# Kernel tuning notes

Measured on AMD Instinct MI355X. Metric: run time of the kernel, lower is better.

Reference implementation:

```python
import jax, jax.numpy as jnp
import numpy as np

N = 768       # num nodes
E = 12288     # num edges (avg degree 16)
D_IN = 6
H = 256       # hidden_dim
TEMPERATURE = 1.0


def gcn_conv(x, W, b, src, dst, n):
    """PyG GCNConv: add self-loops, symmetric deg^-1/2 normalization, then xW aggregation + bias."""
    h = x @ W  # [n, H]
    loop = jnp.arange(n, dtype=src.dtype)
    s = jnp.concatenate([src, loop])
    d = jnp.concatenate([dst, loop])
    deg = jax.ops.segment_sum(jnp.ones(s.shape, dtype=h.dtype), d, num_segments=n)
    dinv = jnp.where(deg > 0, jax.lax.rsqrt(deg), 0.0)
    norm = dinv[s] * dinv[d]  # [E+n]
    out = jax.ops.segment_sum(h[s] * norm[:, None], d, num_segments=n)
    return out + b


def setup_inputs() -> dict:
    key = jax.random.key(0)
    ks = jax.random.split(key, 10)
    sc = lambda fan: np.float32(1.0 / np.sqrt(fan))
    x = jax.random.normal(ks[0], (N, D_IN), jnp.float32)
    edge_index = jax.random.randint(ks[1], (2, E), 0, N, dtype=jnp.int32)
    Wc1 = jax.random.normal(ks[2], (D_IN, H), jnp.float32) * sc(D_IN)
    bc1 = jnp.zeros((H,), jnp.float32)
    Wc2 = jax.random.normal(ks[3], (H, H), jnp.float32) * sc(H)
    bc2 = jnp.zeros((H,), jnp.float32)
    We1 = jax.random.normal(ks[4], (2 * H, H), jnp.float32) * sc(2 * H)
    be1 = jax.random.normal(ks[5], (H,), jnp.float32) * sc(2 * H)
    We2 = jax.random.normal(ks[6], (H, 1), jnp.float32) * sc(H)
    be2 = jax.random.normal(ks[7], (1,), jnp.float32) * sc(H)
    return {"x": x, "edge_index": edge_index, "Wc1": Wc1, "bc1": bc1,
            "Wc2": Wc2, "bc2": bc2, "We1": We1, "be1": be1, "We2": We2, "be2": be2}


def reference(x, edge_index, Wc1, bc1, Wc2, bc2, We1, be1, We2, be2):
    src, dst = edge_index[0], edge_index[1]
    h = jax.nn.elu(gcn_conv(x, Wc1, bc1, src, dst, N))
    h = gcn_conv(h, Wc2, bc2, src, dst, N)  # [N, H]
    # edge scorer: Linear(cat([x_i, x_j])) == x_i @ We1[:H] + x_j @ We1[H:] + be1
    ai = h @ We1[:H]   # [N, H], contribution of x_i (row node)
    aj = h @ We1[H:]   # [N, H], contribution of x_j (col node)
    pair = jax.nn.relu(ai[:, None, :] + aj[None, :, :] + be1)  # [N, N, H]
    logits = jnp.einsum('ijh,h->ij', pair, We2[:, 0]) + be2[0]  # [N, N]
    logits = logits / TEMPERATURE
    logits = jnp.where(jnp.eye(N, dtype=bool), -jnp.inf, logits)
    return jax.nn.softmax(logits, axis=-1)
```

## Files before the change

### kernel.cpp

```cpp
#include <hip/hip_runtime.h>
#include <math.h>

#define N_NODES 768
#define N_EDGES 12288
#define D_INF 6
#define H 256
#define CAP 128
#define LC 256

__global__ __launch_bounds__(256) void k_prep(
    const float* __restrict__ x, const int* __restrict__ ei,
    const float* __restrict__ Wc1, const float* __restrict__ bc1,
    int* __restrict__ cnt_g, int* __restrict__ slots, float* __restrict__ h1) {
    __shared__ int s_cnt[N_NODES];
    __shared__ int s_list[LC];
    __shared__ int s_nm, s_pos[3];
    __shared__ float s_agg[3][D_INF];
    const int t = threadIdx.x, b = blockIdx.x, v0 = b * 3;
    const int* src = ei;
    const int* dst = ei + N_EDGES;

    for (int v = t; v < N_NODES; v += 256) s_cnt[v] = 0;
    if (t == 0) s_nm = 0;
    if (t < 3) s_pos[t] = 0;
    if (t < 3 * D_INF) ((float*)s_agg)[t] = 0.f;
    __syncthreads();
    for (int e = t; e < N_EDGES; e += 256) {
        int d = dst[e];
        atomicAdd(&s_cnt[d], 1);
        unsigned li = (unsigned)(d - v0);
        if (li < 3u) {
            int p = atomicAdd(&s_nm, 1);
            if (p < LC) s_list[p] = (src[e] << 2) | (int)li;
        }
    }
    __syncthreads();
    const int nm = min(s_nm, LC);
    if (t < 3) cnt_g[v0 + t] = s_cnt[v0 + t];
    for (int m = t; m < nm; m += 256) {
        int pk = s_list[m];
        int s = pk >> 2, li = pk & 3;
        int p = atomicAdd(&s_pos[li], 1);
        if (p < CAP) slots[(v0 + li) * CAP + p] = s;
        float w = rsqrtf((float)(s_cnt[s] + 1)) * rsqrtf((float)(s_cnt[v0 + li] + 1));
        #pragma unroll
        for (int k = 0; k < D_INF; ++k)
            atomicAdd(&s_agg[li][k], w * x[s * D_INF + k]);
    }
    if (t < 3) {
        int v = v0 + t;
        float dv2 = 1.0f / (float)(s_cnt[v] + 1);
        #pragma unroll
        for (int k = 0; k < D_INF; ++k)
            atomicAdd(&s_agg[t][k], dv2 * x[v * D_INF + k]);
    }
    __syncthreads();
    #pragma unroll
    for (int r = 0; r < 3; ++r) {
        float acc = bc1[t];
        #pragma unroll
        for (int k = 0; k < D_INF; ++k)
            acc = fmaf(s_agg[r][k], Wc1[k * H + t], acc);
        h1[(v0 + r) * H + t] = (acc > 0.f) ? acc : expm1f(acc);
    }
}

__global__ __launch_bounds__(256) void k_agg(
    const float* __restrict__ h1, const int* __restrict__ cnt,
    const int* __restrict__ slots, float* __restrict__ agg2) {
    __shared__ int   s_s[CAP];
    __shared__ float s_w[CAP];
    const int v = blockIdx.x, t = threadIdx.x;
    const int c = cnt[v];
    const int cc = min(c, CAP);
    const float dv = rsqrtf((float)(c + 1));
    for (int i = t; i < cc; i += 256) {
        int s = slots[v * CAP + i];
        s_s[i] = s;
        s_w[i] = rsqrtf((float)(cnt[s] + 1)) * dv;
    }
    __syncthreads();
    float acc = dv * dv * h1[v * H + t];
    #pragma unroll 4
    for (int n = 0; n < cc; ++n)
        acc = fmaf(s_w[n], h1[s_s[n] * H + t], acc);
    agg2[v * H + t] = acc;
}

__global__ __launch_bounds__(1024) void k_h2(
    const float* __restrict__ agg2, const float* __restrict__ Wc2,
    const float* __restrict__ bc2, float* __restrict__ h2) {
    __shared__ __align__(16) float s_part[16][3][H];
    const int t = threadIdx.x, b = blockIdx.x;
    const int lane = t & 63, w = t >> 6;
    const int v0 = b * 3, k0 = w * 16;

    float a[3][16];
    #pragma unroll
    for (int r = 0; r < 3; ++r)
        #pragma unroll
        for (int q = 0; q < 4; ++q) {
            float4 v = *(const float4*)(agg2 + (size_t)(v0 + r) * H + k0 + q * 4);
            a[r][q * 4 + 0] = v.x; a[r][q * 4 + 1] = v.y;
            a[r][q * 4 + 2] = v.z; a[r][q * 4 + 3] = v.w;
        }
    float4 c0 = {0.f, 0.f, 0.f, 0.f}, c1 = c0, c2 = c0;
    #pragma unroll
    for (int kk = 0; kk < 16; ++kk) {
        float4 wv = *(const float4*)(Wc2 + (size_t)(k0 + kk) * H + (lane << 2));
        c0.x = fmaf(a[0][kk], wv.x, c0.x); c0.y = fmaf(a[0][kk], wv.y, c0.y);
        c0.z = fmaf(a[0][kk], wv.z, c0.z); c0.w = fmaf(a[0][kk], wv.w, c0.w);
        c1.x = fmaf(a[1][kk], wv.x, c1.x); c1.y = fmaf(a[1][kk], wv.y, c1.y);
        c1.z = fmaf(a[1][kk], wv.z, c1.z); c1.w = fmaf(a[1][kk], wv.w, c1.w);
        c2.x = fmaf(a[2][kk], wv.x, c2.x); c2.y = fmaf(a[2][kk], wv.y, c2.y);
        c2.z = fmaf(a[2][kk], wv.z, c2.z); c2.w = fmaf(a[2][kk], wv.w, c2.w);
    }
    *(float4*)&s_part[w][0][lane << 2] = c0;
    *(float4*)&s_part[w][1][lane << 2] = c1;
    *(float4*)&s_part[w][2][lane << 2] = c2;
    __syncthreads();
    if (t < 3 * H) {
        int r = t >> 8, c = t & 255;
        float v = bc2[c];
        #pragma unroll
        for (int ww = 0; ww < 16; ++ww) v += s_part[ww][r][c];
        h2[(size_t)(v0 + r) * H + c] = v;
    }
}

__global__ __launch_bounds__(1024) void k_ae(
    const float* __restrict__ h2, const float* __restrict__ We1,
    const float* __restrict__ be1, float* __restrict__ aib,
    float* __restrict__ ajcT) {
    __shared__ __align__(16) float s_part[16][6][H];
    const int t = threadIdx.x, b = blockIdx.x;
    const int lane = t & 63, w = t >> 6;
    const int v0 = b * 3, k0 = w * 16;

    float a[3][16];
    #pragma unroll
    for (int r = 0; r < 3; ++r)
        #pragma unroll
        for (int q = 0; q < 4; ++q) {
            float4 v = *(const float4*)(h2 + (size_t)(v0 + r) * H + k0 + q * 4);
            a[r][q * 4 + 0] = v.x; a[r][q * 4 + 1] = v.y;
            a[r][q * 4 + 2] = v.z; a[r][q * 4 + 3] = v.w;
        }
    float4 ca0 = {0.f, 0.f, 0.f, 0.f}, ca1 = ca0, ca2 = ca0;
    float4 cb0 = ca0, cb1 = ca0, cb2 = ca0;
    #pragma unroll
    for (int kk = 0; kk < 16; ++kk) {
        int k = k0 + kk;
        float4 wa = *(const float4*)(We1 + (size_t)k * H + (lane << 2));
        float4 wb = *(const float4*)(We1 + (size_t)(H + k) * H + (lane << 2));
        ca0.x = fmaf(a[0][kk], wa.x, ca0.x); ca0.y = fmaf(a[0][kk], wa.y, ca0.y);
        ca0.z = fmaf(a[0][kk], wa.z, ca0.z); ca0.w = fmaf(a[0][kk], wa.w, ca0.w);
        ca1.x = fmaf(a[1][kk], wa.x, ca1.x); ca1.y = fmaf(a[1][kk], wa.y, ca1.y);
        ca1.z = fmaf(a[1][kk], wa.z, ca1.z); ca1.w = fmaf(a[1][kk], wa.w, ca1.w);
        ca2.x = fmaf(a[2][kk], wa.x, ca2.x); ca2.y = fmaf(a[2][kk], wa.y, ca2.y);
        ca2.z = fmaf(a[2][kk], wa.z, ca2.z); ca2.w = fmaf(a[2][kk], wa.w, ca2.w);
        cb0.x = fmaf(a[0][kk], wb.x, cb0.x); cb0.y = fmaf(a[0][kk], wb.y, cb0.y);
        cb0.z = fmaf(a[0][kk], wb.z, cb0.z); cb0.w = fmaf(a[0][kk], wb.w, cb0.w);
        cb1.x = fmaf(a[1][kk], wb.x, cb1.x); cb1.y = fmaf(a[1][kk], wb.y, cb1.y);
        cb1.z = fmaf(a[1][kk], wb.z, cb1.z); cb1.w = fmaf(a[1][kk], wb.w, cb1.w);
        cb2.x = fmaf(a[2][kk], wb.x, cb2.x); cb2.y = fmaf(a[2][kk], wb.y, cb2.y);
        cb2.z = fmaf(a[2][kk], wb.z, cb2.z); cb2.w = fmaf(a[2][kk], wb.w, cb2.w);
    }
    *(float4*)&s_part[w][0][lane << 2] = ca0;
    *(float4*)&s_part[w][1][lane << 2] = ca1;
    *(float4*)&s_part[w][2][lane << 2] = ca2;
    *(float4*)&s_part[w][3][lane << 2] = cb0;
    *(float4*)&s_part[w][4][lane << 2] = cb1;
    *(float4*)&s_part[w][5][lane << 2] = cb2;
    __syncthreads();
    for (int idx = t; idx < 6 * H; idx += 1024) {
        int q = idx >> 8, c = idx & 255;
        float v = 0.f;
        #pragma unroll
        for (int ww = 0; ww < 16; ++ww) v += s_part[ww][q][c];
        if (q < 3) aib[(size_t)(v0 + q) * H + c] = v;
        else       ajcT[(size_t)c * N_NODES + v0 + (q - 3)] = v + be1[c];
    }
}

__global__ __launch_bounds__(512) void k_pair2(
    const float* __restrict__ aib, const float* __restrict__ ajcT,
    const float* __restrict__ We2, float* __restrict__ out) {
    __shared__ float s_ai[3 * H];
    __shared__ float s_w2[H];
    __shared__ __align__(16) float s_p[8 * 3 * N_NODES];
    __shared__ float s_lg[3 * N_NODES];
    __shared__ float red[3 * 256];
    const int t = threadIdx.x, b = blockIdx.x;
    const int lane = t & 63, w = t >> 6;
    const int i0 = b * 3, h0 = w * 32;

    for (int i = t; i < 3 * H; i += 512)
        s_ai[i] = aib[(size_t)(i0 + (i >> 8)) * H + (i & 255)];
    if (t < H) s_w2[t] = We2[t];
    __syncthreads();

    float4 acc[3][3];
    #pragma unroll
    for (int r = 0; r < 3; ++r)
        #pragma unroll
        for (int jj = 0; jj < 3; ++jj)
            acc[r][jj] = make_float4(0.f, 0.f, 0.f, 0.f);

    #pragma unroll 4
    for (int hh = 0; hh < 32; ++hh) {
        int h = h0 + hh;
        float wv = s_w2[h];
        float a0 = s_ai[h], a1 = s_ai[H + h], a2 = s_ai[2 * H + h];
        const float* col = ajcT + (size_t)h * N_NODES + (lane << 2);
        #pragma unroll
        for (int jj = 0; jj < 3; ++jj) {
            float4 bv = *(const float4*)(col + jj * 256);
            acc[0][jj].x = fmaf(fmaxf(a0 + bv.x, 0.f), wv, acc[0][jj].x);
            acc[0][jj].y = fmaf(fmaxf(a0 + bv.y, 0.f), wv, acc[0][jj].y);
            acc[0][jj].z = fmaf(fmaxf(a0 + bv.z, 0.f), wv, acc[0][jj].z);
            acc[0][jj].w = fmaf(fmaxf(a0 + bv.w, 0.f), wv, acc[0][jj].w);
            acc[1][jj].x = fmaf(fmaxf(a1 + bv.x, 0.f), wv, acc[1][jj].x);
            acc[1][jj].y = fmaf(fmaxf(a1 + bv.y, 0.f), wv, acc[1][jj].y);
            acc[1][jj].z = fmaf(fmaxf(a1 + bv.z, 0.f), wv, acc[1][jj].z);
            acc[1][jj].w = fmaf(fmaxf(a1 + bv.w, 0.f), wv, acc[1][jj].w);
            acc[2][jj].x = fmaf(fmaxf(a2 + bv.x, 0.f), wv, acc[2][jj].x);
            acc[2][jj].y = fmaf(fmaxf(a2 + bv.y, 0.f), wv, acc[2][jj].y);
            acc[2][jj].z = fmaf(fmaxf(a2 + bv.z, 0.f), wv, acc[2][jj].z);
            acc[2][jj].w = fmaf(fmaxf(a2 + bv.w, 0.f), wv, acc[2][jj].w);
        }
    }
    #pragma unroll
    for (int r = 0; r < 3; ++r)
        #pragma unroll
        for (int jj = 0; jj < 3; ++jj)
            *(float4*)&s_p[(w * 3 + r) * N_NODES + jj * 256 + (lane << 2)] = acc[r][jj];
    __syncthreads();

    for (int idx = t; idx < 3 * N_NODES; idx += 512) {
        int r = idx / N_NODES, j = idx - r * N_NODES;
        float v = 0.f;
        #pragma unroll
        for (int ww = 0; ww < 8; ++ww) v += s_p[(ww * 3 + r) * N_NODES + j];
        s_lg[idx] = (j == i0 + r) ? -INFINITY : v;
    }
    __syncthreads();

    const int tc = t & 255, th = t >> 8;
    if (th == 0) {
        red[tc] = fmaxf(fmaxf(s_lg[tc], s_lg[tc + 256]), s_lg[tc + 512]);
        red[512 + tc] = fmaxf(fmaxf(s_lg[1536 + tc], s_lg[1536 + tc + 256]),
                              s_lg[1536 + tc + 512]);
    } else {
        red[256 + tc] = fmaxf(fmaxf(s_lg[768 + tc], s_lg[768 + tc + 256]),
                              s_lg[768 + tc + 512]);
    }
    __syncthreads();
    for (int s = 128; s > 0; s >>= 1) {
        if (th == 0 && tc < s) {
            red[tc] = fmaxf(red[tc], red[tc + s]);
            red[512 + tc] = fmaxf(red[512 + tc], red[512 + tc + s]);
        } else if (th == 1 && tc < s) {
            red[256 + tc] = fmaxf(red[256 + tc], red[256 + tc + s]);
        }
        __syncthreads();
    }
    float mx0 = red[0], mx1 = red[256], mx2 = red[512];
    __syncthreads();
    if (th == 0) {
        red[tc] = __expf(s_lg[tc] - mx0) + __expf(s_lg[tc + 256] - mx0)
                + __expf(s_lg[tc + 512] - mx0);
        red[512 + tc] = __expf(s_lg[1536 + tc] - mx2) + __expf(s_lg[1536 + tc + 256] - mx2)
                      + __expf(s_lg[1536 + tc + 512] - mx2);
    } else {
        red[256 + tc] = __expf(s_lg[768 + tc] - mx1) + __expf(s_lg[768 + tc + 256] - mx1)
                      + __expf(s_lg[768 + tc + 512] - mx1);
    }
    __syncthreads();
    for (int s = 128; s > 0; s >>= 1) {
        if (th == 0 && tc < s) {
            red[tc] += red[tc + s];
            red[512 + tc] += red[512 + tc + s];
        } else if (th == 1 && tc < s) {
            red[256 + tc] += red[256 + tc + s];
        }
        __syncthreads();
    }
    float iv0 = 1.0f / red[0], iv1 = 1.0f / red[256], iv2 = 1.0f / red[512];

    for (int idx = t; idx < 3 * N_NODES; idx += 512) {
        int r = idx / N_NODES, j = idx - r * N_NODES;
        float m = (r == 0) ? mx0 : (r == 1) ? mx1 : mx2;
        float iv = (r == 0) ? iv0 : (r == 1) ? iv1 : iv2;
        out[(size_t)(i0 + r) * N_NODES + j] = __expf(s_lg[idx] - m) * iv;
    }
}

extern "C" void kernel_launch(void* const* d_in, const int* in_sizes, int n_in,
                              void* d_out, int out_size, void* d_ws, size_t ws_size,
                              hipStream_t stream) {
    const float* x   = (const float*)d_in[0];
    const int*   ei  = (const int*)d_in[1];
    const float* Wc1 = (const float*)d_in[2];
    const float* bc1 = (const float*)d_in[3];
    const float* Wc2 = (const float*)d_in[4];
    const float* bc2 = (const float*)d_in[5];
    const float* We1 = (const float*)d_in[6];
    const float* be1 = (const float*)d_in[7];
    const float* We2 = (const float*)d_in[8];
    float* out = (float*)d_out;

    char* ws = (char*)d_ws;
    int*   cnt  = (int*)(ws + 0);
    int*   slots= (int*)(ws + 4096);
    float* h1   = (float*)(ws + 397312);
    float* agg2 = (float*)(ws + 1183744);
    float* h2   = (float*)(ws + 1970176);
    float* aib  = (float*)(ws + 2756608);
    float* ajcT = (float*)(ws + 3543040);

    k_prep<<<N_NODES / 3, 256, 0, stream>>>(x, ei, Wc1, bc1, cnt, slots, h1);
    k_agg<<<N_NODES, 256, 0, stream>>>(h1, cnt, slots, agg2);
    k_h2<<<N_NODES / 3, 1024, 0, stream>>>(agg2, Wc2, bc2, h2);
    k_ae<<<N_NODES / 3, 1024, 0, stream>>>(h2, We1, be1, aib, ajcT);
    k_pair2<<<N_NODES / 3, 512, 0, stream>>>(aib, ajcT, We2, out);
}
```

Before: 54.68 us.

## Fuse aggregation, Wc2 GEMM and edge projection into one kernel

Merges the second-layer neighbor aggregation, the Wc2 matmul and the We1 projections into a single kernel with 1024 threads per block, each block handling 3 nodes. Intermediates (aggregated features and h2) stay in shared memory instead of going through global buffers. This removes two kernel launches and the global round trips for agg2 and h2. In exchange, the aggregation phase now runs with only 768 of 1024 threads active and 256 blocks instead of 768, and shared memory use per block grows.

```diff
diff --git a/kernel.cpp b/kernel.cpp
--- a/kernel.cpp
+++ b/kernel.cpp
@@ -65,121 +65,131 @@
     }
 }
 
-__global__ __launch_bounds__(256) void k_agg(
+__global__ __launch_bounds__(1024) void k_mid(
     const float* __restrict__ h1, const int* __restrict__ cnt,
-    const int* __restrict__ slots, float* __restrict__ agg2) {
-    __shared__ int   s_s[CAP];
-    __shared__ float s_w[CAP];
-    const int v = blockIdx.x, t = threadIdx.x;
-    const int c = cnt[v];
-    const int cc = min(c, CAP);
-    const float dv = rsqrtf((float)(c + 1));
-    for (int i = t; i < cc; i += 256) {
-        int s = slots[v * CAP + i];
-        s_s[i] = s;
-        s_w[i] = rsqrtf((float)(cnt[s] + 1)) * dv;
-    }
-    __syncthreads();
-    float acc = dv * dv * h1[v * H + t];
-    #pragma unroll 4
-    for (int n = 0; n < cc; ++n)
-        acc = fmaf(s_w[n], h1[s_s[n] * H + t], acc);
-    agg2[v * H + t] = acc;
-}
-
-__global__ __launch_bounds__(1024) void k_h2(
-    const float* __restrict__ agg2, const float* __restrict__ Wc2,
-    const float* __restrict__ bc2, float* __restrict__ h2) {
-    __shared__ __align__(16) float s_part[16][3][H];
+    const int* __restrict__ slots, const float* __restrict__ Wc2,
+    const float* __restrict__ bc2, const float* __restrict__ We1,
+    const float* __restrict__ be1, float* __restrict__ aib,
+    float* __restrict__ ajcT) {
+    __shared__ int   s_s[3][CAP];
+    __shared__ float s_w[3][CAP];
+    __shared__ int   s_cc[3];
+    __shared__ float s_dv[3];
+    __shared__ __align__(16) float s_agg[3][H];
+    __shared__ __align__(16) float s_h2[3][H];
+    __shared__ __align__(16) float s_part[16][6][H];
     const int t = threadIdx.x, b = blockIdx.x;
+    const int q = t >> 8, tc = t & 255;
     const int lane = t & 63, w = t >> 6;
     const int v0 = b * 3, k0 = w * 16;
 
-    float a[3][16];
-    #pragma unroll
-    for (int r = 0; r < 3; ++r)
-        #pragma unroll
-        for (int q = 0; q < 4; ++q) {
-            float4 v = *(const float4*)(agg2 + (size_t)(v0 + r) * H + k0 + q * 4);
-            a[r][q * 4 + 0] = v.x; a[r][q * 4 + 1] = v.y;
-            a[r][q * 4 + 2] = v.z; a[r][q * 4 + 3] = v.w;
-        }
-    float4 c0 = {0.f, 0.f, 0.f, 0.f}, c1 = c0, c2 = c0;
-    #pragma unroll
-    for (int kk = 0; kk < 16; ++kk) {
-        float4 wv = *(const float4*)(Wc2 + (size_t)(k0 + kk) * H + (lane << 2));
-        c0.x = fmaf(a[0][kk], wv.x, c0.x); c0.y = fmaf(a[0][kk], wv.y, c0.y);
-        c0.z = fmaf(a[0][kk], wv.z, c0.z); c0.w = fmaf(a[0][kk], wv.w, c0.w);
-        c1.x = fmaf(a[1][kk], wv.x, c1.x); c1.y = fmaf(a[1][kk], wv.y, c1.y);
-        c1.z = fmaf(a[1][kk], wv.z, c1.z); c1.w = fmaf(a[1][kk], wv.w, c1.w);
-        c2.x = fmaf(a[2][kk], wv.x, c2.x); c2.y = fmaf(a[2][kk], wv.y, c2.y);
-        c2.z = fmaf(a[2][kk], wv.z, c2.z); c2.w = fmaf(a[2][kk], wv.w, c2.w);
-    }
-    *(float4*)&s_part[w][0][lane << 2] = c0;
-    *(float4*)&s_part[w][1][lane << 2] = c1;
-    *(float4*)&s_part[w][2][lane << 2] = c2;
+    if (t < 3) {
+        int c = cnt[v0 + t];
+        s_cc[t] = min(c, CAP);
+        s_dv[t] = rsqrtf((float)(c + 1));
+    }
+    __syncthreads();
+    if (q < 3) {
+        int ccq = s_cc[q];
+        for (int i = tc; i < ccq; i += 256) {
+            int s = slots[(v0 + q) * CAP + i];
+            s_s[q][i] = s;
+            s_w[q][i] = rsqrtf((float)(cnt[s] + 1)) * s_dv[q];
+        }
+    }
+    __syncthreads();
+
+    if (q < 3) {
+        float dv = s_dv[q];
+        float acc = dv * dv * h1[(size_t)(v0 + q) * H + tc];
+        int ccq = s_cc[q];
+        #pragma unroll 4
+        for (int n = 0; n < ccq; ++n)
+            acc = fmaf(s_w[q][n], h1[(size_t)s_s[q][n] * H + tc], acc);
+        s_agg[q][tc] = acc;
+    }
+    __syncthreads();
+
+    {
+        float a[3][16];
+        #pragma unroll
+        for (int r = 0; r < 3; ++r)
+            #pragma unroll
+            for (int qq = 0; qq < 4; ++qq) {
+                float4 v = *(const float4*)&s_agg[r][k0 + qq * 4];
+                a[r][qq * 4 + 0] = v.x; a[r][qq * 4 + 1] = v.y;
+                a[r][qq * 4 + 2] = v.z; a[r][qq * 4 + 3] = v.w;
+            }
+        float4 c0 = {0.f, 0.f, 0.f, 0.f}, c1 = c0, c2 = c0;
+        #pragma unroll
+        for (int kk = 0; kk < 16; ++kk) {
+            float4 wv = *(const float4*)(Wc2 + (size_t)(k0 + kk) * H + (lane << 2));
+            c0.x = fmaf(a[0][kk], wv.x, c0.x); c0.y = fmaf(a[0][kk], wv.y, c0.y);
+            c0.z = fmaf(a[0][kk], wv.z, c0.z); c0.w = fmaf(a[0][kk], wv.w, c0.w);
+            c1.x = fmaf(a[1][kk], wv.x, c1.x); c1.y = fmaf(a[1][kk], wv.y, c1.y);
+            c1.z = fmaf(a[1][kk], wv.z, c1.z); c1.w = fmaf(a[1][kk], wv.w, c1.w);
+            c2.x = fmaf(a[2][kk], wv.x, c2.x); c2.y = fmaf(a[2][kk], wv.y, c2.y);
+            c2.z = fmaf(a[2][kk], wv.z, c2.z); c2.w = fmaf(a[2][kk], wv.w, c2.w);
+        }
+        *(float4*)&s_part[w][0][lane << 2] = c0;
+        *(float4*)&s_part[w][1][lane << 2] = c1;
+        *(float4*)&s_part[w][2][lane << 2] = c2;
+    }
     __syncthreads();
     if (t < 3 * H) {
         int r = t >> 8, c = t & 255;
         float v = bc2[c];
         #pragma unroll
         for (int ww = 0; ww < 16; ++ww) v += s_part[ww][r][c];
-        h2[(size_t)(v0 + r) * H + c] = v;
-    }
-}
-
-__global__ __launch_bounds__(1024) void k_ae(
-    const float* __restrict__ h2, const float* __restrict__ We1,
-    const float* __restrict__ be1, float* __restrict__ aib,
-    float* __restrict__ ajcT) {
-    __shared__ __align__(16) float s_part[16][6][H];
-    const int t = threadIdx.x, b = blockIdx.x;
-    const int lane = t & 63, w = t >> 6;
-    const int v0 = b * 3, k0 = w * 16;
-
-    float a[3][16];
-    #pragma unroll
-    for (int r = 0; r < 3; ++r)
-        #pragma unroll
-        for (int q = 0; q < 4; ++q) {
-            float4 v = *(const float4*)(h2 + (size_t)(v0 + r) * H + k0 + q * 4);
-            a[r][q * 4 + 0] = v.x; a[r][q * 4 + 1] = v.y;
-            a[r][q * 4 + 2] = v.z; a[r][q * 4 + 3] = v.w;
-        }
-    float4 ca0 = {0.f, 0.f, 0.f, 0.f}, ca1 = ca0, ca2 = ca0;
-    float4 cb0 = ca0, cb1 = ca0, cb2 = ca0;
-    #pragma unroll
-    for (int kk = 0; kk < 16; ++kk) {
-        int k = k0 + kk;
-        float4 wa = *(const float4*)(We1 + (size_t)k * H + (lane << 2));
-        float4 wb = *(const float4*)(We1 + (size_t)(H + k) * H + (lane << 2));
-        ca0.x = fmaf(a[0][kk], wa.x, ca0.x); ca0.y = fmaf(a[0][kk], wa.y, ca0.y);
-        ca0.z = fmaf(a[0][kk], wa.z, ca0.z); ca0.w = fmaf(a[0][kk], wa.w, ca0.w);
-        ca1.x = fmaf(a[1][kk], wa.x, ca1.x); ca1.y = fmaf(a[1][kk], wa.y, ca1.y);
-        ca1.z = fmaf(a[1][kk], wa.z, ca1.z); ca1.w = fmaf(a[1][kk], wa.w, ca1.w);
-        ca2.x = fmaf(a[2][kk], wa.x, ca2.x); ca2.y = fmaf(a[2][kk], wa.y, ca2.y);
-        ca2.z = fmaf(a[2][kk], wa.z, ca2.z); ca2.w = fmaf(a[2][kk], wa.w, ca2.w);
-        cb0.x = fmaf(a[0][kk], wb.x, cb0.x); cb0.y = fmaf(a[0][kk], wb.y, cb0.y);
-        cb0.z = fmaf(a[0][kk], wb.z, cb0.z); cb0.w = fmaf(a[0][kk], wb.w, cb0.w);
-        cb1.x = fmaf(a[1][kk], wb.x, cb1.x); cb1.y = fmaf(a[1][kk], wb.y, cb1.y);
-        cb1.z = fmaf(a[1][kk], wb.z, cb1.z); cb1.w = fmaf(a[1][kk], wb.w, cb1.w);
-        cb2.x = fmaf(a[2][kk], wb.x, cb2.x); cb2.y = fmaf(a[2][kk], wb.y, cb2.y);
-        cb2.z = fmaf(a[2][kk], wb.z, cb2.z); cb2.w = fmaf(a[2][kk], wb.w, cb2.w);
-    }
-    *(float4*)&s_part[w][0][lane << 2] = ca0;
-    *(float4*)&s_part[w][1][lane << 2] = ca1;
-    *(float4*)&s_part[w][2][lane << 2] = ca2;
-    *(float4*)&s_part[w][3][lane << 2] = cb0;
-    *(float4*)&s_part[w][4][lane << 2] = cb1;
-    *(float4*)&s_part[w][5][lane << 2] = cb2;
+        s_h2[r][c] = v;
+    }
+    __syncthreads();
+
+    {
+        float a[3][16];
+        #pragma unroll
+        for (int r = 0; r < 3; ++r)
+            #pragma unroll
+            for (int qq = 0; qq < 4; ++qq) {
+                float4 v = *(const float4*)&s_h2[r][k0 + qq * 4];
+                a[r][qq * 4 + 0] = v.x; a[r][qq * 4 + 1] = v.y;
+                a[r][qq * 4 + 2] = v.z; a[r][qq * 4 + 3] = v.w;
+            }
+        float4 ca0 = {0.f, 0.f, 0.f, 0.f}, ca1 = ca0, ca2 = ca0;
+        float4 cb0 = ca0, cb1 = ca0, cb2 = ca0;
+        #pragma unroll
+        for (int kk = 0; kk < 16; ++kk) {
+            int k = k0 + kk;
+            float4 wa = *(const float4*)(We1 + (size_t)k * H + (lane << 2));
+            float4 wb = *(const float4*)(We1 + (size_t)(H + k) * H + (lane << 2));
+            ca0.x = fmaf(a[0][kk], wa.x, ca0.x); ca0.y = fmaf(a[0][kk], wa.y, ca0.y);
+            ca0.z = fmaf(a[0][kk], wa.z, ca0.z); ca0.w = fmaf(a[0][kk], wa.w, ca0.w);
+            ca1.x = fmaf(a[1][kk], wa.x, ca1.x); ca1.y = fmaf(a[1][kk], wa.y, ca1.y);
+            ca1.z = fmaf(a[1][kk], wa.z, ca1.z); ca1.w = fmaf(a[1][kk], wa.w, ca1.w);
+            ca2.x = fmaf(a[2][kk], wa.x, ca2.x); ca2.y = fmaf(a[2][kk], wa.y, ca2.y);
+            ca2.z = fmaf(a[2][kk], wa.z, ca2.z); ca2.w = fmaf(a[2][kk], wa.w, ca2.w);
+            cb0.x = fmaf(a[0][kk], wb.x, cb0.x); cb0.y = fmaf(a[0][kk], wb.y, cb0.y);
+            cb0.z = fmaf(a[0][kk], wb.z, cb0.z); cb0.w = fmaf(a[0][kk], wb.w, cb0.w);
+            cb1.x = fmaf(a[1][kk], wb.x, cb1.x); cb1.y = fmaf(a[1][kk], wb.y, cb1.y);
+            cb1.z = fmaf(a[1][kk], wb.z, cb1.z); cb1.w = fmaf(a[1][kk], wb.w, cb1.w);
+            cb2.x = fmaf(a[2][kk], wb.x, cb2.x); cb2.y = fmaf(a[2][kk], wb.y, cb2.y);
+            cb2.z = fmaf(a[2][kk], wb.z, cb2.z); cb2.w = fmaf(a[2][kk], wb.w, cb2.w);
+        }
+        *(float4*)&s_part[w][0][lane << 2] = ca0;
+        *(float4*)&s_part[w][1][lane << 2] = ca1;
+        *(float4*)&s_part[w][2][lane << 2] = ca2;
+        *(float4*)&s_part[w][3][lane << 2] = cb0;
+        *(float4*)&s_part[w][4][lane << 2] = cb1;
+        *(float4*)&s_part[w][5][lane << 2] = cb2;
+    }
     __syncthreads();
     for (int idx = t; idx < 6 * H; idx += 1024) {
-        int q = idx >> 8, c = idx & 255;
+        int r6 = idx >> 8, c = idx & 255;
         float v = 0.f;
         #pragma unroll
-        for (int ww = 0; ww < 16; ++ww) v += s_part[ww][q][c];
-        if (q < 3) aib[(size_t)(v0 + q) * H + c] = v;
-        else       ajcT[(size_t)c * N_NODES + v0 + (q - 3)] = v + be1[c];
+        for (int ww = 0; ww < 16; ++ww) v += s_part[ww][r6][c];
+        if (r6 < 3) aib[(size_t)(v0 + r6) * H + c] = v;
+        else        ajcT[(size_t)c * N_NODES + v0 + (r6 - 3)] = v + be1[c];
     }
 }
 
@@ -314,14 +324,11 @@
     int*   cnt  = (int*)(ws + 0);
     int*   slots= (int*)(ws + 4096);
     float* h1   = (float*)(ws + 397312);
-    float* agg2 = (float*)(ws + 1183744);
-    float* h2   = (float*)(ws + 1970176);
-    float* aib  = (float*)(ws + 2756608);
-    float* ajcT = (float*)(ws + 3543040);
+    float* aib  = (float*)(ws + 1183744);
+    float* ajcT = (float*)(ws + 1970176);
 
     k_prep<<<N_NODES / 3, 256, 0, stream>>>(x, ei, Wc1, bc1, cnt, slots, h1);
-    k_agg<<<N_NODES, 256, 0, stream>>>(h1, cnt, slots, agg2);
-    k_h2<<<N_NODES / 3, 1024, 0, stream>>>(agg2, Wc2, bc2, h2);
-    k_ae<<<N_NODES / 3, 1024, 0, stream>>>(h2, We1, be1, aib, ajcT);
+    k_mid<<<N_NODES / 3, 1024, 0, stream>>>(h1, cnt, slots, Wc2, bc2, We1, be1,
+                                            aib, ajcT);
     k_pair2<<<N_NODES / 3, 512, 0, stream>>>(aib, ajcT, We2, out);
 }
```

Measured after the change: 52.47 us, median of 2. -4.0%, faster.
